# Performance work log

Measured on AMD Instinct MI355X. Metric: run time of the kernel, lower is better.

## Reference

```python
import jax, jax.numpy as jnp
import numpy as np

SR = 48000
NC = 8      # num_cylinders
NH = 64     # num_harmonics
NB = 32     # num_noisebands
B_, T_ = 2, 65536
TWO_PI = 2.0 * np.pi


def _gumbel_softmax_hard(key, logits, tau=1.0):
    g = jax.random.gumbel(key, logits.shape, dtype=logits.dtype)
    y = jax.nn.softmax((logits + g) / tau)
    hard = jax.nn.one_hot(jnp.argmax(y, axis=-1), logits.shape[-1], dtype=y.dtype)
    return hard + y - jax.lax.stop_gradient(y)  # straight-through (hard=True)


def _resonant_activation(x, min_mag):
    return jnp.sign(x) * (min_mag + (1.0 - min_mag) * jnp.abs(jnp.tanh(x)))


def _format_coefficients(one_hot, fb_gain, refl, lowpass, tau):
    shifted = jnp.roll(one_hot, 1, axis=-1)
    refl = jax.nn.sigmoid(refl) if lowpass else jnp.tanh(refl)
    k1 = _resonant_activation(refl[0], tau)
    k2 = _resonant_activation(refl[1], tau)
    a1 = k1 * (1.0 - k2)
    a2 = jnp.clip(k2, -0.999, 0.999)
    a1_bound = 0.999 - jnp.abs(a2)
    a1 = jnp.clip(a1, -a1_bound, a1_bound)
    g = jax.nn.sigmoid(fb_gain[0]) ** 0.45
    return one_hot * (a1 * g) + shifted * (a2 * g)


def _sample_wise_lpc(x, a):
    # All-pole IIR: y[t] = x[t] - sum_{i=1..P} a[t, i-1] * y[t-i]
    # x: (B,T), a: (B,T,P) -> (B,T). Inherently sequential scan over T.
    B, T = x.shape
    P = a.shape[-1]

    def step(buf, inp):          # buf: (B,P) = [y[t-1], ..., y[t-P]]
        xt, at = inp             # (B,), (B,P)
        yt = xt - jnp.sum(at * buf, axis=-1)
        buf = jnp.concatenate([yt[:, None], buf[:, :-1]], axis=1)
        return buf, yt

    buf0 = jnp.zeros((B, P), x.dtype)
    _, y = jax.lax.scan(step, buf0, (x.T, jnp.transpose(a, (1, 0, 2))))
    return y.T


def _resonator(excitation, delay_param, fb_gain, refl, min_delay, max_delay, lowpass, tau, key):
    # excitation: (B,1,T)
    sel = _gumbel_softmax_hard(key, delay_param)                 # (max-min,)
    coeffs = _format_coefficients(sel, fb_gain, refl, lowpass, tau)
    coeffs = jnp.concatenate([jnp.zeros(min_delay, coeffs.dtype), coeffs])  # (max_delay,)
    x = excitation[:, 0, :]
    B, T = x.shape
    a = jnp.broadcast_to(coeffs[None, None, :], (B, T, max_delay))
    return _sample_wise_lpc(x, a)[:, None, :]


def setup_inputs() -> dict:
    key = jax.random.key(0)
    ks = jax.random.split(key, 16)
    inp = {
        'f0': jax.random.uniform(ks[0], (B_, 1, T_), jnp.float32),
        'harmonic_amplitudes': jax.random.uniform(ks[1], (B_, NC * NH, T_), jnp.float32),
        'harmonic_fm': jax.random.uniform(ks[2], (B_, 1, T_), jnp.float32),
        'cylinder_phase_offsets': jax.random.normal(ks[3], (B_, NC, T_), jnp.float32),
        'cylinder_pulse_shapes': jax.random.uniform(ks[4], (B_, 2 * NC, T_), jnp.float32),
        'noisebank_amplitudes': jax.random.uniform(ks[5], (B_, NB, T_), jnp.float32),
        'noise_pulse_shapes': jax.random.uniform(ks[6], (B_, 2, T_), jnp.float32),
        'noise_pulse_gain': jax.random.uniform(ks[7], (B_, 1, T_), jnp.float32),
        'flow_noise_gain': jax.random.uniform(ks[8], (B_, 1, T_), jnp.float32),
        'noise_bands': jax.random.normal(ks[9], (NB, T_), jnp.float32),
        'delay_a': jax.random.normal(ks[10], (125 - 40,), jnp.float32),
        'fbgain_a': jnp.ones((1,), jnp.float32),
        'refl_a': jax.random.normal(ks[11], (2,), jnp.float32),
        'delay_b': jax.random.normal(ks[12], (125 - 40,), jnp.float32),
        'fbgain_b': jnp.ones((1,), jnp.float32),
        'refl_b': jax.random.normal(ks[13], (2,), jnp.float32),
        'delay_c': jax.random.normal(ks[14], (40 - 32,), jnp.float32),
        'fbgain_c': jnp.ones((1,), jnp.float32),
        'refl_c': jax.random.normal(ks[15], (2,), jnp.float32),
    }
    return inp


def reference(f0, harmonic_amplitudes, harmonic_fm, cylinder_phase_offsets,
              cylinder_pulse_shapes, noisebank_amplitudes, noise_pulse_shapes,
              noise_pulse_gain, flow_noise_gain, noise_bands,
              delay_a, fbgain_a, refl_a, delay_b, fbgain_b, refl_b,
              delay_c, fbgain_c, refl_c):
    B, C, T = cylinder_phase_offsets.shape
    firing_order = jnp.array([0, 4, 3, 7, 5, 2, 6, 1], dtype=f0.dtype)[:NC]
    firing_angles = firing_order / NC * TWO_PI                         # (8,)
    power_cycle_phase = jnp.cumsum(TWO_PI * f0 / SR, axis=-1) * 0.5    # (B,1,T)
    cylinder_phases = (power_cycle_phase + firing_angles[None, :, None]) % TWO_PI  # (B,8,T)

    hp = (cylinder_phases / TWO_PI) ** harmonic_fm                     # (B,8,T)
    hp = hp * TWO_PI
    harm_idx = jnp.arange(1, NH + 1, dtype=hp.dtype)
    osc = -jnp.sin(hp[:, :, None, :] * harm_idx[None, None, :, None])  # (B,8,64,T)
    amps = harmonic_amplitudes.reshape(B, NC, NH, T)
    harmonics = jnp.sum(osc * amps, axis=2)                            # (B,8,T)

    cyl_alpha = cylinder_pulse_shapes[:, :NC, :]
    cyl_beta = cylinder_pulse_shapes[:, NC:, :]
    cyl_env = (1.0 - jnp.exp(-cyl_alpha * cylinder_phases)) * jnp.exp(-cyl_beta * cylinder_phases)
    harmonics = harmonics * cyl_env * 10.0

    # NoiseBank: fixed noise bands weighted per-sample and summed over bands
    noise = jnp.einsum('bnt,nt->bt', noisebank_amplitudes, noise_bands)[:, None, :]  # (B,1,T)

    n_alpha = noise_pulse_shapes[:, 0:1, :]
    n_beta = noise_pulse_shapes[:, 1:2, :]
    noise_phase = power_cycle_phase % TWO_PI
    noise_env = (1.0 - jnp.exp(-n_alpha * noise_phase)) * jnp.exp(-n_beta * noise_phase)
    noise_bursts = noise * noise_env * noise_pulse_gain
    flow_noise = noise * flow_noise_gain * 0.3
    turbulence = harmonics * noise * (noise_pulse_gain + flow_noise_gain) * 0.7
    cylinders = harmonics + noise_bursts + flow_noise + turbulence     # (B,8,T)

    bank_a = jnp.sum(cylinders[:, :4, :], axis=1, keepdims=True)       # (B,1,T)
    bank_b = jnp.sum(cylinders[:, 4:, :], axis=1, keepdims=True)

    ka, kb, kc = jax.random.split(jax.random.key(42), 3)
    res_a = _resonator(bank_a, delay_a, fbgain_a, refl_a, 40, 125, False, 0.0, ka)
    res_b = _resonator(bank_b, delay_b, fbgain_b, refl_b, 40, 125, False, 0.0, kb)
    res_c = _resonator(res_a + res_b, delay_c, fbgain_c, refl_c, 32, 40, True, 0.0, kc)
    return jnp.sum(res_c, axis=1, keepdims=True)                       # (B,1,T)
```

## Files before the change

### kernel.cpp

```cpp
#include <hip/hip_runtime.h>
#include <cstdint>
#include <cstddef>

#define T_ 65536

__device__ __forceinline__ void tf2x32(uint32_t k0, uint32_t k1,
                                       uint32_t& x0, uint32_t& x1) {
  const uint32_t ks[3] = {k0, k1, k0 ^ k1 ^ 0x1BD11BDAu};
  const int R[8] = {13, 15, 26, 6, 17, 29, 16, 24};
  x0 += ks[0]; x1 += ks[1];
#pragma unroll
  for (int i = 0; i < 5; ++i) {
#pragma unroll
    for (int j = 0; j < 4; ++j) {
      const int r = R[(i & 1) * 4 + j];
      x0 += x1;
      x1 = (x1 << r) | (x1 >> (32 - r));
      x1 ^= x0;
    }
    x0 += ks[(i + 1) % 3];
    x1 += ks[(i + 2) % 3] + (uint32_t)(i + 1);
  }
}

__device__ __forceinline__ float gumbel_from_bits(uint32_t b) {
  float u = __uint_as_float((b >> 9) | 0x3f800000u) - 1.0f;
  u = fmaxf(u, 1.17549435e-38f);
  return -logf(-logf(u));
}

__global__ __launch_bounds__(128) void coef_kernel(
    const float* __restrict__ da, const float* __restrict__ fa, const float* __restrict__ ra,
    const float* __restrict__ db, const float* __restrict__ fb, const float* __restrict__ rb,
    const float* __restrict__ dc, const float* __restrict__ fc, const float* __restrict__ rc,
    float* __restrict__ cws) {
  __shared__ float z[128];
  uint32_t keys[3][2];
#pragma unroll
  for (int q = 0; q < 3; ++q) {
    uint32_t x0 = 0u, x1 = (uint32_t)q;
    tf2x32(0u, 42u, x0, x1);
    keys[q][0] = x0; keys[q][1] = x1;
  }
  const float* dl[3] = {da, db, dc};
  const float* fg[3] = {fa, fb, fc};
  const float* rf[3] = {ra, rb, rc};
  const int Ls[3] = {85, 85, 8};
  const int md[3] = {40, 40, 32};
  const int i = threadIdx.x;
  for (int r = 0; r < 3; ++r) {
    const int L = Ls[r];
    z[i] = -3.4e38f;
    __syncthreads();
    if (i < L) {
      uint32_t x0 = 0u, x1 = (uint32_t)i;
      tf2x32(keys[r][0], keys[r][1], x0, x1);
      z[i] = dl[r][i] + gumbel_from_bits(x0 ^ x1);
    }
    __syncthreads();
    if (i == 0) {
      int p = 0; float best = z[0];
      for (int j = 1; j < L; ++j) { float v = z[j]; if (v > best) { best = v; p = j; } }
      const bool lowpass = (r == 2);
      float r0 = rf[r][0], r1 = rf[r][1];
      if (lowpass) { r0 = 1.f / (1.f + expf(-r0)); r1 = 1.f / (1.f + expf(-r1)); }
      else         { r0 = tanhf(r0);               r1 = tanhf(r1); }
      const float k1 = tanhf(r0), k2 = tanhf(r1);
      float a1 = k1 * (1.f - k2);
      const float a2 = fminf(fmaxf(k2, -0.999f), 0.999f);
      const float bnd = 0.999f - fabsf(a2);
      a1 = fminf(fmaxf(a1, -bnd), bnd);
      const float g = powf(1.f / (1.f + expf(-fg[r][0])), 0.45f);
      const int D1 = md[r] + p + 1;
      const int D2 = md[r] + ((p + 1) % L) + 1;
      const float C1 = a1 * g;
      const float C2 = a2 * g;
      float* cw = cws + r * 32;
      const float bin4[5] = {1.f, 4.f, 6.f, 4.f, 1.f};
      const float c1p[5] = {1.f, C1, C1*C1, C1*C1*C1, C1*C1*C1*C1};
      const float c2p[5] = {1.f, C2, C2*C2, C2*C2*C2, C2*C2*C2*C2};
      for (int j = 0; j < 5; ++j) {
        cw[j]     = (float)((4 - j) * D1 + j * D2);
        cw[5 + j] = bin4[j] * c1p[4 - j] * c2p[j];
      }
      const int   fd[9] = {D1, D2, 2*D1, D1+D2, 2*D2, 3*D1, 2*D1+D2, D1+2*D2, 3*D2};
      const float fn[9] = {-C1, -C2, C1*C1, 2.f*C1*C2, C2*C2,
                           -C1*C1*C1, -3.f*C1*C1*C2, -3.f*C1*C2*C2, -C2*C2*C2};
      for (int k = 0; k < 9; ++k) {
        cw[10 + k] = (float)fd[k];
        cw[19 + k] = fn[k];
      }
    }
    __syncthreads();
  }
}

__global__ __launch_bounds__(1024) void pcp_kernel(const float* __restrict__ f0,
                                                   float* __restrict__ pcp) {
  __shared__ double sm[1024];
  const int b = blockIdx.x;
  const int tid = threadIdx.x;
  const float* src = f0 + (size_t)b * T_;
  const int base = tid * 64;
  double loc = 0.0;
  for (int k = 0; k < 64; ++k) {
    loc += 6.283185307179586 * (double)src[base + k] / 48000.0;
  }
  sm[tid] = loc;
  __syncthreads();
  for (int off = 1; off < 1024; off <<= 1) {
    double v = (tid >= off) ? sm[tid - off] : 0.0;
    __syncthreads();
    sm[tid] += v;
    __syncthreads();
  }
  double run = (tid > 0) ? sm[tid - 1] : 0.0;
  float* dst = pcp + (size_t)b * T_;
  for (int k = 0; k < 64; ++k) {
    run += 6.283185307179586 * (double)src[base + k] / 48000.0;
    dst[base + k] = (float)(run * 0.5);
  }
}

__global__ __launch_bounds__(256) void synth_kernel(
    const float* __restrict__ amps,
    const float* __restrict__ fmg,
    const float* __restrict__ cps,
    const float* __restrict__ nba,
    const float* __restrict__ nps,
    const float* __restrict__ npg,
    const float* __restrict__ fng,
    const float* __restrict__ bands,
    const float* __restrict__ pcp,
    float* __restrict__ bank_a, float* __restrict__ bank_b) {
  const float TPF = 6.283185307179586f;
  const int gid = blockIdx.x * 256 + threadIdx.x;
  const int b = gid >> 15;
  const int t = (gid & 32767) * 2;
  const size_t bt = (size_t)b * T_ + t;
  const float p0 = pcp[bt], p1 = pcp[bt + 1];
  const float fm0 = fmg[bt], fm1 = fmg[bt + 1];

  float nse0 = 0.f, nse1 = 0.f;
  for (int n = 0; n < 32; ++n) {
    const float2 a = *(const float2*)(nba + ((size_t)b * 32 + n) * T_ + t);
    const float2 w = *(const float2*)(bands + (size_t)n * T_ + t);
    nse0 += a.x * w.x; nse1 += a.y * w.y;
  }

  const int order[8] = {0, 4, 3, 7, 5, 2, 6, 1};
  float ha0 = 0, ha1 = 0, hb0 = 0, hb1 = 0;
#pragma unroll
  for (int c = 0; c < 8; ++c) {
    const float ang = ((float)order[c] / 8.0f) * TPF;
    float s0 = p0 + ang; if (s0 >= TPF) s0 -= TPF;
    float s1 = p1 + ang; if (s1 >= TPF) s1 -= TPF;
    const float th0 = TPF * powf(s0 / TPF, fm0);
    const float th1 = TPF * powf(s1 / TPF, fm1);
    float sn0, cs0, sn1, cs1;
    sincosf(th0, &sn0, &cs0);
    sincosf(th1, &sn1, &cs1);
    float sp0 = 0.f, sc0 = sn0, sp1 = 0.f, sc1 = sn1;
    const float tc0 = 2.f * cs0, tc1 = 2.f * cs1;
    float acc0 = 0.f, acc1 = 0.f;
    const float* ap = amps + ((size_t)b * 512 + (size_t)c * 64) * T_ + t;
#pragma unroll 4
    for (int h = 0; h < 64; ++h) {
      const float2 a = *(const float2*)(ap + (size_t)h * T_);
      acc0 += a.x * sc0; acc1 += a.y * sc1;
      const float nx0 = tc0 * sc0 - sp0; sp0 = sc0; sc0 = nx0;
      const float nx1 = tc1 * sc1 - sp1; sp1 = sc1; sc1 = nx1;
    }
    const float2 al = *(const float2*)(cps + ((size_t)b * 16 + c) * T_ + t);
    const float2 be = *(const float2*)(cps + ((size_t)b * 16 + 8 + c) * T_ + t);
    const float env0 = (1.f - expf(-al.x * s0)) * expf(-be.x * s0);
    const float env1 = (1.f - expf(-al.y * s1)) * expf(-be.y * s1);
    const float hh0 = -acc0 * env0 * 10.f;
    const float hh1 = -acc1 * env1 * 10.f;
    if (c < 4) { ha0 += hh0; ha1 += hh1; } else { hb0 += hh0; hb1 += hh1; }
  }

  const float g0 = npg[bt], g1 = npg[bt + 1];
  const float fl0 = fng[bt], fl1 = fng[bt + 1];
  const float na0 = nps[(size_t)b * 2 * T_ + t],     na1 = nps[(size_t)b * 2 * T_ + t + 1];
  const float nb0 = nps[((size_t)b * 2 + 1) * T_ + t], nb1 = nps[((size_t)b * 2 + 1) * T_ + t + 1];
  float q0 = p0; if (q0 >= TPF) q0 -= TPF;
  float q1 = p1; if (q1 >= TPF) q1 -= TPF;
  const float ne0 = (1.f - expf(-na0 * q0)) * expf(-nb0 * q0);
  const float ne1 = (1.f - expf(-na1 * q1)) * expf(-nb1 * q1);
  const float com0 = nse0 * (ne0 * g0 + fl0 * 0.3f);
  const float com1 = nse1 * (ne1 * g1 + fl1 * 0.3f);
  const float K0 = nse0 * (g0 + fl0) * 0.7f;
  const float K1 = nse1 * (g1 + fl1) * 0.7f;
  *(float2*)(bank_a + bt) = make_float2(ha0 * (1.f + K0) + 4.f * com0,
                                        ha1 * (1.f + K1) + 4.f * com1);
  *(float2*)(bank_b + bt) = make_float2(hb0 * (1.f + K0) + 4.f * com0,
                                        hb1 * (1.f + K1) + 4.f * com1);
}

__global__ __launch_bounds__(256) void prep_ab_kernel(
    const float* __restrict__ BA, const float* __restrict__ BB,
    const float* __restrict__ CW, float* __restrict__ XA, float* __restrict__ XB) {
  const int idx = blockIdx.x * 256 + threadIdx.x;
  const int t = idx & (T_ - 1);
  const int s = idx >> 16;
  const int r = s >> 1, b = s & 1;
  const float* xin = (r == 0 ? BA : BB) + (size_t)b * T_;
  float* xout = (r == 0 ? XA : XB) + (size_t)b * T_;
  const float* cw = CW + r * 32;
  float acc = xin[t];
#pragma unroll
  for (int k = 0; k < 9; ++k) {
    const int d = (int)cw[10 + k];
    const float n = cw[19 + k];
    const int tc = t - d;
    const float u = xin[tc >= 0 ? tc : 0];
    acc += (tc >= 0) ? n * u : 0.f;
  }
  xout[t] = acc;
}

__global__ __launch_bounds__(256) void prep_c_kernel(
    const float* __restrict__ RA, const float* __restrict__ RB,
    const float* __restrict__ CW, float* __restrict__ XC) {
  const int idx = blockIdx.x * 256 + threadIdx.x;
  const int t = idx & (T_ - 1);
  const int b = idx >> 16;
  const float* ya = RA + (size_t)b * T_;
  const float* yb = RB + (size_t)b * T_;
  const float* cw = CW + 64;
  float acc = ya[t] + yb[t];
#pragma unroll
  for (int k = 0; k < 9; ++k) {
    const int d = (int)cw[10 + k];
    const float n = cw[19 + k];
    const int tc = t - d;
    const float u = ya[tc >= 0 ? tc : 0] + yb[tc >= 0 ? tc : 0];
    acc += (tc >= 0) ? n * u : 0.f;
  }
  XC[idx] = acc;
}

__device__ __forceinline__ void gld16(const float* g, float* l) {
  __builtin_amdgcn_global_load_lds((const __attribute__((address_space(1))) void*)g,
                                   (__attribute__((address_space(3))) void*)l, 16, 0, 0);
}

__device__ __forceinline__ void poly_scan(const float* __restrict__ x,
                                          float* __restrict__ y,
                                          const float* __restrict__ cf,
                                          float* __restrict__ sm) {
  const int o = threadIdx.x & 63;
  const int e0 = (int)cf[0], e1 = (int)cf[1], e2 = (int)cf[2],
            e3 = (int)cf[3], e4 = (int)cf[4];
  const float fc0 = cf[5], fc1 = cf[6], fc2 = cf[7], fc3 = cf[8], fc4 = cf[9];
  float* ring = sm;
  float* st   = sm + 1024;

#pragma unroll
  for (int i = 0; i < 16; ++i) ring[o + i * 64] = 0.f;

  {
    const float* g = x + (o << 2);
    gld16(g, st); gld16(g + 256, st + 256);
    gld16(g + 512, st + 512); gld16(g + 768, st + 768);
  }

  float a0 = ring[(o - e0) & 1023];
  float a1v = ring[(o - e1) & 1023];
  float a2v = ring[(o - e2) & 1023];
  float a3v = ring[(o - e3) & 1023];
  float a4v = ring[(o - e4) & 1023];
  float b0 = ring[(o + 64 - e0) & 1023];
  float b1v = ring[(o + 64 - e1) & 1023];
  float b2v = ring[(o + 64 - e2) & 1023];
  float b3v = ring[(o + 64 - e3) & 1023];
  float b4v = ring[(o + 64 - e4) & 1023];

  int t = o;
  for (int ph = 0; ph < 64; ++ph) {
    const int q = ph & 1;
    asm volatile("s_waitcnt vmcnt(0)" ::: "memory");
    if (ph < 63) {
      const float* g = x + (ph + 1) * 1024 + (o << 2);
      float* l = st + (q ^ 1) * 1024;
      gld16(g, l); gld16(g + 256, l + 256);
      gld16(g + 512, l + 512); gld16(g + 768, l + 768);
    }
    const float* bq = st + q * 1024;
    float xv0 = bq[o];
    float xv1 = bq[64 + o];
#pragma unroll
    for (int l = 0; l < 16; l += 2) {
      {
        const float s01 = fmaf(fc0, a0, fc1 * a1v);
        const float s23 = fmaf(fc2, a2v, fc3 * a3v);
        const float yv = xv0 + (s01 + fmaf(fc4, a4v, s23));
        ring[t & 1023] = yv;
        y[t] = yv;
        a0  = ring[(t + 128 - e0) & 1023];
        a1v = ring[(t + 128 - e1) & 1023];
        a2v = ring[(t + 128 - e2) & 1023];
        a3v = ring[(t + 128 - e3) & 1023];
        a4v = ring[(t + 128 - e4) & 1023];
        if (l + 2 < 16) xv0 = bq[(l + 2) * 64 + o];
        t += 64;
      }
      {
        const float s01 = fmaf(fc0, b0, fc1 * b1v);
        const float s23 = fmaf(fc2, b2v, fc3 * b3v);
        const float yv = xv1 + (s01 + fmaf(fc4, b4v, s23));
        ring[t & 1023] = yv;
        y[t] = yv;
        b0  = ring[(t + 128 - e0) & 1023];
        b1v = ring[(t + 128 - e1) & 1023];
        b2v = ring[(t + 128 - e2) & 1023];
        b3v = ring[(t + 128 - e3) & 1023];
        b4v = ring[(t + 128 - e4) & 1023];
        if (l + 3 < 16) xv1 = bq[(l + 3) * 64 + o];
        t += 64;
      }
    }
  }
}

__global__ __launch_bounds__(64) void res_ab_kernel(
    const float* __restrict__ XA, const float* __restrict__ XB,
    float* __restrict__ RA, float* __restrict__ RB, const float* __restrict__ CW) {
  __shared__ float sm[3072];
  const int r = blockIdx.x >> 1;
  const int b = blockIdx.x & 1;
  poly_scan((r == 0 ? XA : XB) + (size_t)b * T_,
            (r == 0 ? RA : RB) + (size_t)b * T_, CW + r * 32, sm);
}

__global__ __launch_bounds__(64) void res_c_kernel(
    const float* __restrict__ XC, float* __restrict__ out,
    const float* __restrict__ CW) {
  __shared__ float sm[3072];
  poly_scan(XC + (size_t)blockIdx.x * T_, out + (size_t)blockIdx.x * T_,
            CW + 64, sm);
}

extern "C" void kernel_launch(void* const* d_in, const int* in_sizes, int n_in,
                              void* d_out, int out_size, void* d_ws, size_t ws_size,
                              hipStream_t stream) {
  const float* f0    = (const float*)d_in[0];
  const float* amps  = (const float*)d_in[1];
  const float* fmg   = (const float*)d_in[2];
  const float* cps   = (const float*)d_in[4];
  const float* nba   = (const float*)d_in[5];
  const float* nps   = (const float*)d_in[6];
  const float* npg   = (const float*)d_in[7];
  const float* fng   = (const float*)d_in[8];
  const float* bands = (const float*)d_in[9];
  const float* da  = (const float*)d_in[10];
  const float* fga = (const float*)d_in[11];
  const float* ra  = (const float*)d_in[12];
  const float* db  = (const float*)d_in[13];
  const float* fgb = (const float*)d_in[14];
  const float* rb  = (const float*)d_in[15];
  const float* dc  = (const float*)d_in[16];
  const float* fgc = (const float*)d_in[17];
  const float* rc  = (const float*)d_in[18];
  float* out = (float*)d_out;
  float* ws  = (float*)d_ws;

  float* S0 = ws;
  float* S1 = ws + 131072;
  float* S2 = ws + 262144;
  float* S3 = ws + 393216;
  float* CW = ws + 524288;

  pcp_kernel<<<2, 1024, 0, stream>>>(f0, S0);
  coef_kernel<<<1, 128, 0, stream>>>(da, fga, ra, db, fgb, rb, dc, fgc, rc, CW);
  synth_kernel<<<256, 256, 0, stream>>>(amps, fmg, cps, nba, nps, npg, fng, bands,
                                        S0, S1, S2);
  prep_ab_kernel<<<1024, 256, 0, stream>>>(S1, S2, CW, S0, S3);
  res_ab_kernel<<<4, 64, 0, stream>>>(S0, S3, S1, S2, CW);
  prep_c_kernel<<<512, 256, 0, stream>>>(S1, S2, CW, S3);
  res_c_kernel<<<2, 64, 0, stream>>>(S3, out, CW);
}
```

Measured before the change: 297.6 us.

## Split synth work across four wavefronts per block with shared-memory reduction

The synth kernel now gives each block 128 time samples and splits the cylinder and noise-band loops across four wavefronts. Each wavefront handles two cylinders and eight noise bands, and the partial sums are combined through LDS. The grid grows from 256 to 1024 blocks, which should raise occupancy and memory-level parallelism on a GPU with many CUs. The cost is a __syncthreads, LDS traffic, and a tail section where only one wavefront per block is active.

```diff
diff --git a/kernel.cpp b/kernel.cpp
--- a/kernel.cpp
+++ b/kernel.cpp
@@ -134,24 +134,34 @@
     const float* __restrict__ pcp,
     float* __restrict__ bank_a, float* __restrict__ bank_b) {
   const float TPF = 6.283185307179586f;
-  const int gid = blockIdx.x * 256 + threadIdx.x;
-  const int b = gid >> 15;
-  const int t = (gid & 32767) * 2;
+  const int lane = threadIdx.x & 63;
+  const int g    = threadIdx.x >> 6;
+  const int blk  = blockIdx.x;
+  const int b    = blk >> 9;
+  const int t    = (blk & 511) * 128 + lane * 2;
   const size_t bt = (size_t)b * T_ + t;
+
+  __shared__ float2 redN[4][64];
+  __shared__ float2 redH[4][64];
+
   const float p0 = pcp[bt], p1 = pcp[bt + 1];
   const float fm0 = fmg[bt], fm1 = fmg[bt + 1];
 
   float nse0 = 0.f, nse1 = 0.f;
-  for (int n = 0; n < 32; ++n) {
+#pragma unroll
+  for (int j = 0; j < 8; ++j) {
+    const int n = g * 8 + j;
     const float2 a = *(const float2*)(nba + ((size_t)b * 32 + n) * T_ + t);
     const float2 w = *(const float2*)(bands + (size_t)n * T_ + t);
     nse0 += a.x * w.x; nse1 += a.y * w.y;
   }
+  redN[g][lane] = make_float2(nse0, nse1);
 
   const int order[8] = {0, 4, 3, 7, 5, 2, 6, 1};
-  float ha0 = 0, ha1 = 0, hb0 = 0, hb1 = 0;
-#pragma unroll
-  for (int c = 0; c < 8; ++c) {
+  float hp0 = 0.f, hp1 = 0.f;
+#pragma unroll
+  for (int cc = 0; cc < 2; ++cc) {
+    const int c = 2 * g + cc;
     const float ang = ((float)order[c] / 8.0f) * TPF;
     float s0 = p0 + ang; if (s0 >= TPF) s0 -= TPF;
     float s1 = p1 + ang; if (s1 >= TPF) s1 -= TPF;
@@ -175,27 +185,39 @@
     const float2 be = *(const float2*)(cps + ((size_t)b * 16 + 8 + c) * T_ + t);
     const float env0 = (1.f - expf(-al.x * s0)) * expf(-be.x * s0);
     const float env1 = (1.f - expf(-al.y * s1)) * expf(-be.y * s1);
-    const float hh0 = -acc0 * env0 * 10.f;
-    const float hh1 = -acc1 * env1 * 10.f;
-    if (c < 4) { ha0 += hh0; ha1 += hh1; } else { hb0 += hh0; hb1 += hh1; }
-  }
-
-  const float g0 = npg[bt], g1 = npg[bt + 1];
-  const float fl0 = fng[bt], fl1 = fng[bt + 1];
-  const float na0 = nps[(size_t)b * 2 * T_ + t],     na1 = nps[(size_t)b * 2 * T_ + t + 1];
-  const float nb0 = nps[((size_t)b * 2 + 1) * T_ + t], nb1 = nps[((size_t)b * 2 + 1) * T_ + t + 1];
-  float q0 = p0; if (q0 >= TPF) q0 -= TPF;
-  float q1 = p1; if (q1 >= TPF) q1 -= TPF;
-  const float ne0 = (1.f - expf(-na0 * q0)) * expf(-nb0 * q0);
-  const float ne1 = (1.f - expf(-na1 * q1)) * expf(-nb1 * q1);
-  const float com0 = nse0 * (ne0 * g0 + fl0 * 0.3f);
-  const float com1 = nse1 * (ne1 * g1 + fl1 * 0.3f);
-  const float K0 = nse0 * (g0 + fl0) * 0.7f;
-  const float K1 = nse1 * (g1 + fl1) * 0.7f;
-  *(float2*)(bank_a + bt) = make_float2(ha0 * (1.f + K0) + 4.f * com0,
-                                        ha1 * (1.f + K1) + 4.f * com1);
-  *(float2*)(bank_b + bt) = make_float2(hb0 * (1.f + K0) + 4.f * com0,
-                                        hb1 * (1.f + K1) + 4.f * com1);
+    hp0 += -acc0 * env0 * 10.f;
+    hp1 += -acc1 * env1 * 10.f;
+  }
+  redH[g][lane] = make_float2(hp0, hp1);
+  __syncthreads();
+
+  if (g == 0) {
+    const float2 n0 = redN[0][lane], n1 = redN[1][lane],
+                 n2 = redN[2][lane], n3 = redN[3][lane];
+    const float nseA = n0.x + n1.x + n2.x + n3.x;
+    const float nseB = n0.y + n1.y + n2.y + n3.y;
+    const float2 h0 = redH[0][lane], h1 = redH[1][lane],
+                 h2 = redH[2][lane], h3 = redH[3][lane];
+    const float ha0 = h0.x + h1.x, ha1 = h0.y + h1.y;
+    const float hb0 = h2.x + h3.x, hb1 = h2.y + h3.y;
+
+    const float g0 = npg[bt], g1 = npg[bt + 1];
+    const float fl0 = fng[bt], fl1 = fng[bt + 1];
+    const float na0 = nps[(size_t)b * 2 * T_ + t],       na1 = nps[(size_t)b * 2 * T_ + t + 1];
+    const float nb0 = nps[((size_t)b * 2 + 1) * T_ + t], nb1 = nps[((size_t)b * 2 + 1) * T_ + t + 1];
+    float q0 = p0; if (q0 >= TPF) q0 -= TPF;
+    float q1 = p1; if (q1 >= TPF) q1 -= TPF;
+    const float ne0 = (1.f - expf(-na0 * q0)) * expf(-nb0 * q0);
+    const float ne1 = (1.f - expf(-na1 * q1)) * expf(-nb1 * q1);
+    const float com0 = nseA * (ne0 * g0 + fl0 * 0.3f);
+    const float com1 = nseB * (ne1 * g1 + fl1 * 0.3f);
+    const float K0 = nseA * (g0 + fl0) * 0.7f;
+    const float K1 = nseB * (g1 + fl1) * 0.7f;
+    *(float2*)(bank_a + bt) = make_float2(ha0 * (1.f + K0) + 4.f * com0,
+                                          ha1 * (1.f + K1) + 4.f * com1);
+    *(float2*)(bank_b + bt) = make_float2(hb0 * (1.f + K0) + 4.f * com0,
+                                          hb1 * (1.f + K1) + 4.f * com1);
+  }
 }
 
 __global__ __launch_bounds__(256) void prep_ab_kernel(
@@ -374,8 +396,8 @@
 
   pcp_kernel<<<2, 1024, 0, stream>>>(f0, S0);
   coef_kernel<<<1, 128, 0, stream>>>(da, fga, ra, db, fgb, rb, dc, fgc, rc, CW);
-  synth_kernel<<<256, 256, 0, stream>>>(amps, fmg, cps, nba, nps, npg, fng, bands,
-                                        S0, S1, S2);
+  synth_kernel<<<1024, 256, 0, stream>>>(amps, fmg, cps, nba, nps, npg, fng, bands,
+                                         S0, S1, S2);
   prep_ab_kernel<<<1024, 256, 0, stream>>>(S1, S2, CW, S0, S3);
   res_ab_kernel<<<4, 64, 0, stream>>>(S0, S3, S1, S2, CW);
   prep_c_kernel<<<512, 256, 0, stream>>>(S1, S2, CW, S3);
```

After: 260.0 us. 12.6% less time.
